# Kernel optimization log

Hardware: AMD Instinct MI355X
Metric: run time of the kernel (lower is better)

Reference implementation:

```python
import jax, jax.numpy as jnp
import numpy as np

N_FEAT = 27  # 26 embeddings + bot MLP output
LI = np.array([i for i in range(N_FEAT) for j in range(i)])
LJ = np.array([j for i in range(N_FEAT) for j in range(i)])


def _mlp(x, Ws, bs):
    for W, b in zip(Ws, bs):
        x = jax.nn.relu(x @ W + b)
    return x


def setup_inputs() -> dict:
    key = jax.random.key(0)
    ks = jax.random.split(key, 32)
    B, V, D = 32768, 50000, 128
    bot = [13, 512, 256, 128]
    top = [479, 1024, 1024, 512, 256, 1]
    inp = {
        "dense_x": jax.random.normal(ks[0], (B, 13), dtype=jnp.float32),
        "sparse_x": jax.random.randint(ks[1], (B, 26), 0, V, dtype=jnp.int64),
        "emb": jax.random.normal(ks[2], (26, V, D), dtype=jnp.float32) * 0.01,
    }
    for i in range(3):
        inp[f"bw{i}"] = jax.random.normal(ks[3 + i], (bot[i], bot[i + 1]), dtype=jnp.float32) * (1.0 / np.sqrt(bot[i]))
        inp[f"bb{i}"] = jnp.zeros((bot[i + 1],), dtype=jnp.float32)
    for i in range(5):
        inp[f"tw{i}"] = jax.random.normal(ks[8 + i], (top[i], top[i + 1]), dtype=jnp.float32) * (1.0 / np.sqrt(top[i]))
        inp[f"tb{i}"] = jnp.zeros((top[i + 1],), dtype=jnp.float32)
    return inp


def reference(dense_x, sparse_x, emb,
              bw0, bb0, bw1, bb1, bw2, bb2,
              tw0, tb0, tw1, tb1, tw2, tb2, tw3, tb3, tw4, tb4):
    B = dense_x.shape[0]
    bot_out = _mlp(dense_x, [bw0, bw1, bw2], [bb0, bb1, bb2])  # [B, 128]
    # multi-table embedding gather: emb[t, sparse_x[:, t]] -> [B, 26, 128]
    gathered = jnp.take_along_axis(
        emb[None, :, :, :],  # broadcast over batch via vmap-style gather
        sparse_x.T[None, :, :, None].astype(jnp.int32) * 0, 0
    ) if False else jnp.stack(
        [emb[t][sparse_x[:, t]] for t in range(emb.shape[0])], axis=1
    )
    features = jnp.concatenate([bot_out[:, None, :], gathered], axis=1)  # [B, 27, 128]
    # batched dot interaction: [B, 27, 27], then triangular gather
    Z = jnp.einsum('bnd,bmd->bnm', features, features)
    interact = Z[:, LI, LJ]  # [B, 351]
    x = jnp.concatenate([bot_out, interact], axis=1)  # [B, 479]
    return _mlp(x, [tw0, tw1, tw2, tw3, tw4], [tb0, tb1, tb2, tb3, tb4])  # [B, 1]
```

## Files before the change

### kernel.cpp

```cpp
#include <hip/hip_runtime.h>

typedef _Float16 f16;
typedef __attribute__((ext_vector_type(2))) _Float16 f16x2;
typedef __attribute__((ext_vector_type(4))) _Float16 f16x4;
typedef __attribute__((ext_vector_type(8))) _Float16 f16x8;
typedef __attribute__((ext_vector_type(4))) float f32x4;

#define BM 128
#define BN 128
#define BK 32

__device__ __forceinline__ void gl_lds16(const void* g, void* l) {
    __builtin_amdgcn_global_load_lds(
        (const __attribute__((address_space(1))) void*)g,
        (__attribute__((address_space(3))) void*)l, 16, 0, 0);
}

struct ConvtDesc { const float* src; f16* dst; int K, N, Kpad, tileOff; };
struct ConvtArgs { ConvtDesc d[6]; };

__global__ void convtbot_kernel(ConvtArgs args, const float* __restrict__ xin,
                                const float* __restrict__ bw0,
                                const float* __restrict__ bb0, f16* __restrict__ act0)
{
    int tid = threadIdx.x;
    if (blockIdx.x >= 584) {
        __shared__ float xs[64][13];
        int rbase = (blockIdx.x - 584) * 64;
        int n0 = tid * 2;
        float wr0[13], wr1[13];
        #pragma unroll
        for (int k = 0; k < 13; ++k) {
            wr0[k] = bw0[k * 512 + n0];
            wr1[k] = bw0[k * 512 + n0 + 1];
        }
        float b0v = bb0[n0], b1v = bb0[n0 + 1];
        for (int t = tid; t < 64 * 13; t += 256)
            xs[t / 13][t % 13] = xin[(size_t)rbase * 13 + t];
        __syncthreads();
        #pragma unroll 4
        for (int r = 0; r < 64; ++r) {
            float a0 = b0v, a1 = b1v;
            #pragma unroll
            for (int k = 0; k < 13; ++k) {
                float xv = xs[r][k];
                a0 += xv * wr0[k];
                a1 += xv * wr1[k];
            }
            f16x2 v;
            v[0] = (f16)fmaxf(a0, 0.f);
            v[1] = (f16)fmaxf(a1, 0.f);
            *(f16x2*)(act0 + (size_t)(rbase + r) * 512 + n0) = v;
        }
        return;
    }
    __shared__ float tile[64][65];
    int bid = blockIdx.x;
    int w = 0;
    #pragma unroll
    for (int i = 1; i < 6; ++i) if (bid >= args.d[i].tileOff) w = i;
    const float* __restrict__ src = args.d[w].src;
    f16* __restrict__ dst = args.d[w].dst;
    int K = args.d[w].K, N = args.d[w].N, Kpad = args.d[w].Kpad;
    int local = bid - args.d[w].tileOff;
    int tk = Kpad >> 6;
    int k0 = (local % tk) * 64;
    int n0 = (local / tk) * 64;
    #pragma unroll
    for (int it = 0; it < 16; ++it) {
        int idx = it * 256 + tid;
        int kr = idx >> 6, nc = idx & 63;
        float v = 0.f;
        if (k0 + kr < K) v = src[(size_t)(k0 + kr) * N + n0 + nc];
        tile[kr][nc] = v;
    }
    __syncthreads();
    #pragma unroll
    for (int it = 0; it < 16; ++it) {
        int idx = it * 256 + tid;
        int nr = idx >> 6, kc = idx & 63;
        dst[(size_t)(n0 + nr) * Kpad + k0 + kc] = (f16)tile[kc][nr];
    }
}

__global__ void gemm_f16(const f16* __restrict__ A, const f16* __restrict__ WT,
                         const float* __restrict__ bias, f16* __restrict__ C,
                         int N, int K,
                         const float* __restrict__ w4, float* __restrict__ partial)
{
    __shared__ __align__(16) f16 sm[16384];
    f16* lsA0 = sm;
    f16* lsB0 = sm + 8192;
    int tid  = threadIdx.x;
    int lane = tid & 63;
    int wave = tid >> 6;
    int brow = blockIdx.y * BM;
    int bcol = blockIdx.x * BN;
    int wr = wave >> 1, wc = wave & 1;

    int rsel = lane & 15;
    int k8   = lane >> 4;

    auto stage = [&](int buf, int kt) {
        int k0 = kt * BK;
        #pragma unroll
        for (int i = 0; i < 2; ++i) {
            int flat = i * 256 + tid;
            int row  = flat >> 2;
            int slot = flat & 3;
            int sg   = slot ^ ((row >> 1) & 3);
            gl_lds16(A  + (size_t)(brow + row) * K + k0 + sg * 8, lsA0 + buf * 4096 + flat * 8);
            gl_lds16(WT + (size_t)(bcol + row) * K + k0 + sg * 8, lsB0 + buf * 4096 + flat * 8);
        }
    };

    int nK = K / BK;
    f32x4 acc[4][4] = {};
    stage(0, 0);
    for (int kt = 0; kt < nK; ++kt) {
        int cur = kt & 1;
        if (kt + 1 < nK) {
            stage(cur ^ 1, kt + 1);
            asm volatile("s_waitcnt vmcnt(4)" ::: "memory");
        } else {
            asm volatile("s_waitcnt vmcnt(0)" ::: "memory");
        }
        __builtin_amdgcn_s_barrier();

        __builtin_amdgcn_s_setprio(1);
        f16x8 aF[4], bF[4];
        #pragma unroll
        for (int m = 0; m < 4; ++m) {
            int ra = wr * 64 + m * 16 + rsel;
            int sa = k8 ^ ((ra >> 1) & 3);
            aF[m] = *(const f16x8*)(lsA0 + cur * 4096 + ra * 32 + sa * 8);
        }
        #pragma unroll
        for (int n = 0; n < 4; ++n) {
            int rb = wc * 64 + n * 16 + rsel;
            int sb = k8 ^ ((rb >> 1) & 3);
            bF[n] = *(const f16x8*)(lsB0 + cur * 4096 + rb * 32 + sb * 8);
        }
        #pragma unroll
        for (int m = 0; m < 4; ++m)
            #pragma unroll
            for (int n = 0; n < 4; ++n)
                acc[m][n] = __builtin_amdgcn_mfma_f32_16x16x32_f16(aF[m], bF[n], acc[m][n], 0, 0, 0);
        __builtin_amdgcn_s_setprio(0);
        asm volatile("s_waitcnt lgkmcnt(0)" ::: "memory");
        __builtin_amdgcn_s_barrier();
    }

    #pragma unroll
    for (int n = 0; n < 4; ++n) {
        int col = wc * 64 + n * 16 + rsel;
        float bv = bias[bcol + col];
        int ch = (col >> 3) ^ (k8 << 2);
        #pragma unroll
        for (int m = 0; m < 4; ++m) {
            int row = wr * 64 + m * 16 + k8 * 4;
            #pragma unroll
            for (int r = 0; r < 4; ++r)
                sm[(row + r) * 128 + ch * 8 + (col & 7)] = (f16)fmaxf(acc[m][n][r] + bv, 0.f);
        }
    }
    __syncthreads();
    if (w4 == nullptr) {
        int ch = tid & 15, r0 = tid >> 4;
        #pragma unroll
        for (int p = 0; p < 8; ++p) {
            int row = r0 + p * 16;
            int sch = ch ^ (((row >> 2) & 3) << 2);
            f16x8 v = *(const f16x8*)(sm + row * 128 + sch * 8);
            *(f16x8*)(C + (size_t)(brow + row) * N + bcol + ch * 8) = v;
        }
    } else {
        int r = tid >> 1, h = tid & 1;
        int s4 = ((r >> 2) & 3) << 2;
        float a2 = 0.f;
        #pragma unroll
        for (int i = 0; i < 8; ++i) {
            int cc = h * 8 + i;
            f16x8 cv = *(const f16x8*)(sm + r * 128 + (cc ^ s4) * 8);
            #pragma unroll
            for (int e = 0; e < 8; ++e)
                a2 += (float)cv[e] * w4[bcol + cc * 8 + e];
        }
        a2 += __shfl_xor(a2, 1, 64);
        if (h == 0) partial[(size_t)(brow + r) * 2 + blockIdx.x] = a2;
    }
}

__global__ void finish_kernel(const float* __restrict__ partial,
                              const float* __restrict__ b4, float* __restrict__ out)
{
    int b = blockIdx.x * 256 + threadIdx.x;
    out[b] = fmaxf(partial[(size_t)b * 2] + partial[(size_t)b * 2 + 1] + b4[0], 0.f);
}

#define VM(n) asm volatile("s_waitcnt vmcnt(" #n ")" ::: "memory")
#define LGKM0 asm volatile("s_waitcnt lgkmcnt(0)" ::: "memory")

#define DSREAD_A(MH)                                                            \
    {                                                                           \
        const f16* pA = ls + cb * 32768 + (MH * 2) * 8192;                      \
        _Pragma("unroll")                                                       \
        for (int m = 0; m < 4; ++m) {                                           \
            int ra = wmq * 64 + m * 16 + rsel;                                  \
            _Pragma("unroll")                                                   \
            for (int ks = 0; ks < 2; ++ks) {                                    \
                int s = (ks * 4 + k8) ^ (ra & 7);                               \
                aF[m][ks] = *(const f16x8*)(pA + ra * 64 + s * 8);              \
            }                                                                   \
        }                                                                       \
    }

#define DSREAD_B(NH)                                                            \
    {                                                                           \
        const f16* pB = ls + cb * 32768 + (NH * 2 + 1) * 8192;                  \
        _Pragma("unroll")                                                       \
        for (int n = 0; n < 2; ++n) {                                           \
            int rb = wnq * 32 + n * 16 + rsel;                                  \
            _Pragma("unroll")                                                   \
            for (int ks = 0; ks < 2; ++ks) {                                    \
                int s = (ks * 4 + k8) ^ (rb & 7);                               \
                bF[NH][n][ks] = *(const f16x8*)(pB + rb * 64 + s * 8);          \
            }                                                                   \
        }                                                                       \
    }

#define MFMAQ(q, NH)                                                            \
    __builtin_amdgcn_s_barrier();                                               \
    __builtin_amdgcn_s_setprio(1);                                              \
    _Pragma("unroll")                                                           \
    for (int m = 0; m < 4; ++m)                                                 \
        _Pragma("unroll")                                                       \
        for (int n = 0; n < 2; ++n)                                             \
            _Pragma("unroll")                                                   \
            for (int ks = 0; ks < 2; ++ks)                                      \
                acc[q][m][n] = __builtin_amdgcn_mfma_f32_16x16x32_f16(          \
                    aF[m][ks], bF[NH][n][ks], acc[q][m][n], 0, 0, 0);           \
    __builtin_amdgcn_s_setprio(0);

__global__ __launch_bounds__(512, 2) void gemm256_8ph(
    const f16* __restrict__ A, const f16* __restrict__ WT,
    const float* __restrict__ bias, f16* __restrict__ C, int N, int K)
{
    __shared__ __align__(16) f16 ls[2 * 4 * 128 * 64];
    int tid  = threadIdx.x;
    int lane = tid & 63;
    int wid  = tid >> 6;
    int wmq = wid >> 2, wnq = wid & 3;

    int nbx = gridDim.x;
    int flat = blockIdx.y * nbx + blockIdx.x;
    int nchunk = (nbx * gridDim.y) >> 3;
    int nf = (flat & 7) * nchunk + (flat >> 3);
    int bx = nf % nbx, by = nf / nbx;
    int brow = by * 256, bcol = bx * 256;

    int rsel = lane & 15;
    int k8   = lane >> 4;
    const size_t szK = (size_t)K;

    auto stage_half = [&](int dbuf, int hreg, int kt) {
        const f16* mat = (hreg & 1) ? WT : A;
        int base = (hreg & 1) ? bcol : brow;
        const f16* g = mat + (size_t)(base + (hreg >> 1) * 128) * szK + kt * 64;
        f16* d = ls + dbuf * 32768 + hreg * 8192;
        #pragma unroll
        for (int i = 0; i < 2; ++i) {
            int fl  = i * 512 + tid;
            int row = fl >> 3, sl = fl & 7;
            int sg  = sl ^ (row & 7);
            gl_lds16(g + (size_t)row * szK + sg * 8, d + fl * 8);
        }
    };

    int nK = K / 64;
    f32x4 acc[4][4][2] = {};

    stage_half(0, 0, 0); stage_half(0, 1, 0);
    stage_half(0, 3, 0); stage_half(0, 2, 0);
    VM(2);
    __builtin_amdgcn_s_barrier();

    for (int kt = 0; kt < nK; ++kt) {
        int cb = kt & 1, nb = cb ^ 1;
        bool nl = (kt + 1 < nK);
        f16x8 aF[4][2], bF[2][2][2];
        DSREAD_A(0)
        DSREAD_B(0)
        DSREAD_B(1)
        if (nl) stage_half(nb, 0, kt + 1);
        MFMAQ(0, 0)
        __builtin_amdgcn_s_barrier();
        if (nl) { stage_half(nb, 1, kt + 1); VM(4); } else { VM(0); }
        MFMAQ(1, 1)
        __builtin_amdgcn_s_barrier();
        DSREAD_A(1)
        if (nl) stage_half(nb, 3, kt + 1);
        MFMAQ(2, 1)
        __builtin_amdgcn_s_barrier();
        if (nl) { stage_half(nb, 2, kt + 1); VM(2); }
        MFMAQ(3, 0)
        LGKM0;
        __builtin_amdgcn_s_barrier();
    }

    const int mhq[4] = {0, 0, 1, 1};
    const int nhq[4] = {0, 1, 1, 0};
    #pragma unroll
    for (int q = 0; q < 4; ++q) {
        #pragma unroll
        for (int n = 0; n < 2; ++n) {
            int col = nhq[q] * 128 + wnq * 32 + n * 16 + rsel;
            float bv = bias[bcol + col];
            int ch = (col >> 3) ^ (k8 << 2);
            #pragma unroll
            for (int m = 0; m < 4; ++m) {
                int row = mhq[q] * 128 + wmq * 64 + m * 16 + k8 * 4;
                #pragma unroll
                for (int r = 0; r < 4; ++r)
                    ls[(row + r) * 256 + ch * 8 + (col & 7)] = (f16)fmaxf(acc[q][m][n][r] + bv, 0.f);
            }
        }
    }
    __syncthreads();
    {
        int ch = tid & 31, r0 = tid >> 5;
        #pragma unroll
        for (int p = 0; p < 16; ++p) {
            int row = r0 + p * 16;
            int sch = ch ^ (((row >> 2) & 3) << 2);
            f16x8 v = *(const f16x8*)(ls + row * 256 + sch * 8);
            *(f16x8*)(C + (size_t)(brow + row) * N + bcol + ch * 8) = v;
        }
    }
}

__global__ void interact_mfma(const f16* __restrict__ botout,
                              const float* __restrict__ emb,
                              const int* __restrict__ sparse,
                              f16* __restrict__ x, int V)
{
    __shared__ __align__(16) f16 F[4][32][128];
    int tid  = threadIdx.x;
    int lane = tid & 63, wave = tid >> 6;
    int b0 = blockIdx.x * 4;
    f16* xs_w = &F[wave][27][0];

    for (int t = tid; t < 4 * 27 * 16; t += 256) {
        int s   = t / (27 * 16);
        int rem = t - s * (27 * 16);
        int r   = rem >> 4;
        int c   = rem & 15;
        int b   = b0 + s;
        f16x8 v;
        if (r == 0) {
            v = *(const f16x8*)(botout + (size_t)b * 128 + c * 8);
        } else {
            const f32x4* src = (const f32x4*)(emb + ((size_t)(r - 1) * V + sparse[b * 26 + (r - 1)]) * 128 + c * 8);
            f32x4 u0 = src[0], u1 = src[1];
            #pragma unroll
            for (int e = 0; e < 4; ++e) { v[e] = (f16)u0[e]; v[4 + e] = (f16)u1[e]; }
        }
        *(f16x8*)(&F[s][r][(c ^ (r & 15)) * 8]) = v;
    }
    if (tid < 4 * 33) {
        int s = tid / 33;
        (&F[s][27][0])[479 + tid % 33] = (f16)0;
    }
    __syncthreads();

    f32x4 a00 = {}, a10 = {}, a11 = {};
    int rl = lane & 15, ch = lane >> 4;
    #pragma unroll
    for (int ks = 0; ks < 4; ++ks) {
        int c = ks * 4 + ch;
        f16x8 f0 = *(const f16x8*)(&F[wave][rl]     [(c ^ rl) * 8]);
        f16x8 f1 = *(const f16x8*)(&F[wave][16 + rl][(c ^ rl) * 8]);
        a00 = __builtin_amdgcn_mfma_f32_16x16x32_f16(f0, f0, a00, 0, 0, 0);
        a10 = __builtin_amdgcn_mfma_f32_16x16x32_f16(f1, f0, a10, 0, 0, 0);
        a11 = __builtin_amdgcn_mfma_f32_16x16x32_f16(f1, f1, a11, 0, 0, 0);
    }

    #pragma unroll
    for (int r = 0; r < 4; ++r) {
        int i = ch * 4 + r, j = rl;
        if (i > j) xs_w[128 + (i * (i - 1)) / 2 + j] = (f16)a00[r];
    }
    #pragma unroll
    for (int r = 0; r < 4; ++r) {
        int i = 16 + ch * 4 + r, j = rl;
        if (i < 27) xs_w[128 + (i * (i - 1)) / 2 + j] = (f16)a10[r];
    }
    #pragma unroll
    for (int r = 0; r < 4; ++r) {
        int i = 16 + ch * 4 + r, j = 16 + rl;
        if (i < 27 && j < i) xs_w[128 + (i * (i - 1)) / 2 + j] = (f16)a11[r];
    }
    #pragma unroll
    for (int d = lane; d < 128; d += 64) xs_w[d] = F[wave][0][d];
    __syncthreads();

    {
        int b = b0 + wave;
        f16x8 v = *(const f16x8*)(&xs_w[lane * 8]);
        *(f16x8*)(x + (size_t)b * 512 + lane * 8) = v;
    }
}

extern "C" void kernel_launch(void* const* d_in, const int* in_sizes, int n_in,
                              void* d_out, int out_size, void* d_ws, size_t ws_size,
                              hipStream_t stream)
{
    (void)n_in; (void)out_size; (void)ws_size;
    const float* dense  = (const float*)d_in[0];
    const int*   sparse = (const int*)  d_in[1];
    const float* emb    = (const float*)d_in[2];
    const float* bw0 = (const float*)d_in[3];
    const float* bb0 = (const float*)d_in[4];
    const float* bw1 = (const float*)d_in[5];
    const float* bb1 = (const float*)d_in[6];
    const float* bw2 = (const float*)d_in[7];
    const float* bb2 = (const float*)d_in[8];
    const float* tw0 = (const float*)d_in[9];
    const float* tb0 = (const float*)d_in[10];
    const float* tw1 = (const float*)d_in[11];
    const float* tb1 = (const float*)d_in[12];
    const float* tw2 = (const float*)d_in[13];
    const float* tb2 = (const float*)d_in[14];
    const float* tw3 = (const float*)d_in[15];
    const float* tb3 = (const float*)d_in[16];
    const float* tw4 = (const float*)d_in[17];
    const float* tb4 = (const float*)d_in[18];
    float* out = (float*)d_out;

    const int B = in_sizes[0] / 13;
    const int V = in_sizes[2] / (26 * 128);

    char* ws = (char*)d_ws;
    size_t off = 0;
    auto alloc = [&](size_t bytes) {
        char* p = ws + off;
        off += (bytes + 255) & ~(size_t)255;
        return p;
    };
    f16* S1   = (f16*)alloc((size_t)B * 1024 * 2);
    f16* t1   = (f16*)alloc((size_t)B * 1024 * 2);
    f16* S3   = (f16*)alloc((size_t)B * 512 * 2);
    f16* S4   = (f16*)alloc((size_t)B * 256 * 2);
    f16* act2 = (f16*)alloc((size_t)B * 128 * 2);
    float* partial = (float*)alloc((size_t)B * 2 * 4);
    f16* bw1T = (f16*)alloc((size_t)256 * 512 * 2);
    f16* bw2T = (f16*)alloc((size_t)128 * 256 * 2);
    f16* tw0T = (f16*)alloc((size_t)1024 * 512 * 2);
    f16* tw1T = (f16*)alloc((size_t)1024 * 1024 * 2);
    f16* tw2T = (f16*)alloc((size_t)512 * 1024 * 2);
    f16* tw3T = (f16*)alloc((size_t)256 * 512 * 2);
    f16* act0 = S1; f16* t2 = S1;
    f16* x    = S3; f16* t3 = S3;
    f16* act1 = S4;

    ConvtArgs ca;
    ca.d[0] = { bw1, bw1T,  512,  256,  512,   0 };
    ca.d[1] = { bw2, bw2T,  256,  128,  256,  32 };
    ca.d[2] = { tw0, tw0T,  479, 1024,  512,  40 };
    ca.d[3] = { tw1, tw1T, 1024, 1024, 1024, 168 };
    ca.d[4] = { tw2, tw2T, 1024,  512, 1024, 424 };
    ca.d[5] = { tw3, tw3T,  512,  256,  512, 552 };
    convtbot_kernel<<<584 + B / 64, 256, 0, stream>>>(ca, dense, bw0, bb0, act0);

    gemm_f16<<<dim3( 256/128, B/128), 256, 0, stream>>>(act0, bw1T, bb1, act1,  256,  512, nullptr, nullptr);
    gemm_f16<<<dim3( 128/128, B/128), 256, 0, stream>>>(act1, bw2T, bb2, act2,  128,  256, nullptr, nullptr);
    interact_mfma<<<B / 4, 256, 0, stream>>>(act2, emb, sparse, x, V);
    gemm256_8ph<<<dim3(1024/256, B/256), 512, 0, stream>>>(x,  tw0T, tb0, t1, 1024,  512);
    gemm256_8ph<<<dim3(1024/256, B/256), 512, 0, stream>>>(t1, tw1T, tb1, t2, 1024, 1024);
    gemm256_8ph<<<dim3( 512/256, B/256), 512, 0, stream>>>(t2, tw2T, tb2, t3,  512, 1024);
    gemm_f16<<<dim3( 256/128, B/128), 256, 0, stream>>>(t3, tw3T, tb3, nullptr, 256, 512, tw4, partial);
    finish_kernel<<<B / 256, 256, 0, stream>>>(partial, tb4, out);
}
```

Baseline: 346.3 us.

## Switch 256x256 GEMM to 32x32x16 MFMA with two-phase schedule

Replaces the 16x16x32 MFMA inner loop with 32x32x16 MFMA tiles. Each wave now owns a 64-column slab of B that it reads once per K-step, and the K-step is reorganised from four quadrant phases into two M-half phases. The larger MFMA shape is meant to cut LDS fragment reads per FLOP and the number of barriers per K iteration. In exchange, load/compute overlap is coarser (two stage_half calls per phase), and the epilogue has to be remapped to the 32x32 accumulator layout.

```diff
diff --git a/kernel.cpp b/kernel.cpp
--- a/kernel.cpp
+++ b/kernel.cpp
@@ -5,6 +5,7 @@
 typedef __attribute__((ext_vector_type(4))) _Float16 f16x4;
 typedef __attribute__((ext_vector_type(8))) _Float16 f16x8;
 typedef __attribute__((ext_vector_type(4))) float f32x4;
+typedef __attribute__((ext_vector_type(16))) float f32x16;
 
 #define BM 128
 #define BN 128
@@ -201,47 +202,6 @@
 #define VM(n) asm volatile("s_waitcnt vmcnt(" #n ")" ::: "memory")
 #define LGKM0 asm volatile("s_waitcnt lgkmcnt(0)" ::: "memory")
 
-#define DSREAD_A(MH)                                                            \
-    {                                                                           \
-        const f16* pA = ls + cb * 32768 + (MH * 2) * 8192;                      \
-        _Pragma("unroll")                                                       \
-        for (int m = 0; m < 4; ++m) {                                           \
-            int ra = wmq * 64 + m * 16 + rsel;                                  \
-            _Pragma("unroll")                                                   \
-            for (int ks = 0; ks < 2; ++ks) {                                    \
-                int s = (ks * 4 + k8) ^ (ra & 7);                               \
-                aF[m][ks] = *(const f16x8*)(pA + ra * 64 + s * 8);              \
-            }                                                                   \
-        }                                                                       \
-    }
-
-#define DSREAD_B(NH)                                                            \
-    {                                                                           \
-        const f16* pB = ls + cb * 32768 + (NH * 2 + 1) * 8192;                  \
-        _Pragma("unroll")                                                       \
-        for (int n = 0; n < 2; ++n) {                                           \
-            int rb = wnq * 32 + n * 16 + rsel;                                  \
-            _Pragma("unroll")                                                   \
-            for (int ks = 0; ks < 2; ++ks) {                                    \
-                int s = (ks * 4 + k8) ^ (rb & 7);                               \
-                bF[NH][n][ks] = *(const f16x8*)(pB + rb * 64 + s * 8);          \
-            }                                                                   \
-        }                                                                       \
-    }
-
-#define MFMAQ(q, NH)                                                            \
-    __builtin_amdgcn_s_barrier();                                               \
-    __builtin_amdgcn_s_setprio(1);                                              \
-    _Pragma("unroll")                                                           \
-    for (int m = 0; m < 4; ++m)                                                 \
-        _Pragma("unroll")                                                       \
-        for (int n = 0; n < 2; ++n)                                             \
-            _Pragma("unroll")                                                   \
-            for (int ks = 0; ks < 2; ++ks)                                      \
-                acc[q][m][n] = __builtin_amdgcn_mfma_f32_16x16x32_f16(          \
-                    aF[m][ks], bF[NH][n][ks], acc[q][m][n], 0, 0, 0);           \
-    __builtin_amdgcn_s_setprio(0);
-
 __global__ __launch_bounds__(512, 2) void gemm256_8ph(
     const f16* __restrict__ A, const f16* __restrict__ WT,
     const float* __restrict__ bias, f16* __restrict__ C, int N, int K)
@@ -251,6 +211,7 @@
     int lane = tid & 63;
     int wid  = tid >> 6;
     int wmq = wid >> 2, wnq = wid & 3;
+    int l31 = lane & 31, h = lane >> 5;
 
     int nbx = gridDim.x;
     int flat = blockIdx.y * nbx + blockIdx.x;
@@ -259,8 +220,6 @@
     int bx = nf % nbx, by = nf / nbx;
     int brow = by * 256, bcol = bx * 256;
 
-    int rsel = lane & 15;
-    int k8   = lane >> 4;
     const size_t szK = (size_t)K;
 
     auto stage_half = [&](int dbuf, int hreg, int kt) {
@@ -278,7 +237,10 @@
     };
 
     int nK = K / 64;
-    f32x4 acc[4][4][2] = {};
+    f32x16 acc[2][2][2] = {};
+    f16x8 bF[2][4];
+    int bregion = 1 + ((wnq >> 1) << 1);
+    int broff0 = (wnq & 1) * 64;
 
     stage_half(0, 0, 0); stage_half(0, 1, 0);
     stage_half(0, 3, 0); stage_half(0, 2, 0);
@@ -288,44 +250,86 @@
     for (int kt = 0; kt < nK; ++kt) {
         int cb = kt & 1, nb = cb ^ 1;
         bool nl = (kt + 1 < nK);
-        f16x8 aF[4][2], bF[2][2][2];
-        DSREAD_A(0)
-        DSREAD_B(0)
-        DSREAD_B(1)
-        if (nl) stage_half(nb, 0, kt + 1);
-        MFMAQ(0, 0)
-        __builtin_amdgcn_s_barrier();
-        if (nl) { stage_half(nb, 1, kt + 1); VM(4); } else { VM(0); }
-        MFMAQ(1, 1)
-        __builtin_amdgcn_s_barrier();
-        DSREAD_A(1)
-        if (nl) stage_half(nb, 3, kt + 1);
-        MFMAQ(2, 1)
-        __builtin_amdgcn_s_barrier();
-        if (nl) { stage_half(nb, 2, kt + 1); VM(2); }
-        MFMAQ(3, 0)
+        f16x8 aF[2][4];
+        {
+            const f16* pA = ls + cb * 32768 + 0 * 8192;
+            #pragma unroll
+            for (int m = 0; m < 2; ++m) {
+                int roff = wmq * 64 + m * 32 + l31;
+                #pragma unroll
+                for (int kk = 0; kk < 4; ++kk) {
+                    int s = (kk * 2 + h) ^ (roff & 7);
+                    aF[m][kk] = *(const f16x8*)(pA + roff * 64 + s * 8);
+                }
+            }
+            const f16* pB = ls + cb * 32768 + bregion * 8192;
+            #pragma unroll
+            for (int n = 0; n < 2; ++n) {
+                int roff = broff0 + n * 32 + l31;
+                #pragma unroll
+                for (int kk = 0; kk < 4; ++kk) {
+                    int s = (kk * 2 + h) ^ (roff & 7);
+                    bF[n][kk] = *(const f16x8*)(pB + roff * 64 + s * 8);
+                }
+            }
+        }
+        if (nl) { stage_half(nb, 0, kt + 1); stage_half(nb, 1, kt + 1); VM(4); }
+        else    { VM(0); }
+        __builtin_amdgcn_s_barrier();
+        __builtin_amdgcn_s_setprio(1);
+        #pragma unroll
+        for (int kk = 0; kk < 4; ++kk)
+            #pragma unroll
+            for (int m = 0; m < 2; ++m)
+                #pragma unroll
+                for (int n = 0; n < 2; ++n)
+                    acc[0][m][n] = __builtin_amdgcn_mfma_f32_32x32x16_f16(
+                        aF[m][kk], bF[n][kk], acc[0][m][n], 0, 0, 0);
+        __builtin_amdgcn_s_setprio(0);
+        __builtin_amdgcn_s_barrier();
+        {
+            const f16* pA = ls + cb * 32768 + 2 * 8192;
+            #pragma unroll
+            for (int m = 0; m < 2; ++m) {
+                int roff = wmq * 64 + m * 32 + l31;
+                #pragma unroll
+                for (int kk = 0; kk < 4; ++kk) {
+                    int s = (kk * 2 + h) ^ (roff & 7);
+                    aF[m][kk] = *(const f16x8*)(pA + roff * 64 + s * 8);
+                }
+            }
+        }
+        if (nl) { stage_half(nb, 3, kt + 1); stage_half(nb, 2, kt + 1); VM(2); }
+        __builtin_amdgcn_s_barrier();
+        __builtin_amdgcn_s_setprio(1);
+        #pragma unroll
+        for (int kk = 0; kk < 4; ++kk)
+            #pragma unroll
+            for (int m = 0; m < 2; ++m)
+                #pragma unroll
+                for (int n = 0; n < 2; ++n)
+                    acc[1][m][n] = __builtin_amdgcn_mfma_f32_32x32x16_f16(
+                        aF[m][kk], bF[n][kk], acc[1][m][n], 0, 0, 0);
+        __builtin_amdgcn_s_setprio(0);
         LGKM0;
         __builtin_amdgcn_s_barrier();
     }
 
-    const int mhq[4] = {0, 0, 1, 1};
-    const int nhq[4] = {0, 1, 1, 0};
-    #pragma unroll
-    for (int q = 0; q < 4; ++q) {
-        #pragma unroll
-        for (int n = 0; n < 2; ++n) {
-            int col = nhq[q] * 128 + wnq * 32 + n * 16 + rsel;
-            float bv = bias[bcol + col];
-            int ch = (col >> 3) ^ (k8 << 2);
-            #pragma unroll
-            for (int m = 0; m < 4; ++m) {
-                int row = mhq[q] * 128 + wmq * 64 + m * 16 + k8 * 4;
-                #pragma unroll
-                for (int r = 0; r < 4; ++r)
-                    ls[(row + r) * 256 + ch * 8 + (col & 7)] = (f16)fmaxf(acc[q][m][n][r] + bv, 0.f);
+    #pragma unroll
+    for (int mh = 0; mh < 2; ++mh)
+        #pragma unroll
+        for (int m = 0; m < 2; ++m)
+            #pragma unroll
+            for (int n = 0; n < 2; ++n) {
+                int col = wnq * 64 + n * 32 + l31;
+                float bv = bias[bcol + col];
+                #pragma unroll
+                for (int r = 0; r < 16; ++r) {
+                    int row = mh * 128 + wmq * 64 + m * 32 + (r & 3) + 8 * (r >> 2) + 4 * h;
+                    int ch = (col >> 3) ^ (((row >> 2) & 3) << 2);
+                    ls[row * 256 + ch * 8 + (col & 7)] = (f16)fmaxf(acc[mh][m][n][r] + bv, 0.f);
+                }
             }
-        }
-    }
     __syncthreads();
     {
         int ch = tid & 31, r0 = tid >> 5;
```

New measurement: 377.6 us. 1.09x slower.
